# Optimization experiments

Measured on AMD Instinct MI355X. Metric: run time of the kernel, lower is better.

## Reference

```python
import jax, jax.numpy as jnp
import numpy as np

NUM_HEADS = 32  # head_dim = input_dim // num_heads = 32 == C (forced by matmul contraction)


def setup_inputs() -> dict:
    key = jax.random.key(0)
    ks = jax.random.split(key, 8)
    B, C, D3, H1 = 16, 32, 1, 32
    input_dim = 1024  # == C**2, forced by the final view(B, C, H1, W1)
    s = 0.02
    x1 = jax.random.normal(ks[0], (B, C, D3, H1, input_dim), jnp.float32)
    x2 = jax.random.normal(ks[1], (B, C, D3, H1, input_dim), jnp.float32)
    Wq = jax.random.normal(ks[2], (input_dim, input_dim), jnp.float32) * s
    bq = jax.random.normal(ks[3], (input_dim,), jnp.float32) * s
    Wk = jax.random.normal(ks[4], (input_dim, input_dim), jnp.float32) * s
    bk = jax.random.normal(ks[5], (input_dim,), jnp.float32) * s
    Wv = jax.random.normal(ks[6], (input_dim, input_dim), jnp.float32) * s
    bv = jax.random.normal(ks[7], (input_dim,), jnp.float32) * s
    return {"x1": x1, "x2": x2, "Wq": Wq, "bq": bq, "Wk": Wk, "bk": bk, "Wv": Wv, "bv": bv}


def reference(x1, x2, Wq, bq, Wk, bk, Wv, bv):
    B, C, _, H1, W1 = x1.shape  # W1 == input_dim (Linear acts on last dim)
    nh = NUM_HEADS
    hd = W1 // nh
    # Linear projections on the last axis (torch Linear: x @ W.T + b)
    q = (x1 @ Wq.T + bq).reshape(B, C, nh, hd, -1).transpose(0, 2, 4, 3, 1)  # (B, nh, L1, hd, C)
    k = (x2 @ Wk.T + bk).reshape(B, C, nh, hd, -1)                            # (B, C, nh, hd, L2)
    v = (x2 @ Wv.T + bv).reshape(B, C, nh, hd, -1)                            # (B, C, nh, hd, L2)
    # Broadcasted batched matmul: contracts q's trailing C axis with k's hd axis (C == hd).
    energy = jnp.matmul(q, k)                      # (B, C, L1, hd, L2)
    attention = jax.nn.softmax(energy, axis=-1)    # softmax over L2
    # Contracts v's L2 axis with attention's hd axis (L2 == hd).
    out = jnp.matmul(v, attention)                 # (B, C, L1, hd, L2)
    out = out.transpose(0, 2, 4, 3, 1).reshape(B, C, H1, W1)
    return out
```

## Files before the change

kernel.cpp:

```cpp
#include <hip/hip_runtime.h>
#include <cstdint>

typedef __bf16 bf16x8 __attribute__((ext_vector_type(8)));
typedef float f32x4 __attribute__((ext_vector_type(4)));
typedef unsigned short us8 __attribute__((ext_vector_type(8)));

__device__ __forceinline__ unsigned short f2bf(float f) {
  union { float f; uint32_t u; } c; c.f = f;
  uint32_t u = c.u + 0x7FFFu + ((c.u >> 16) & 1u);
  return (unsigned short)(u >> 16);
}
__device__ __forceinline__ float bf2f(unsigned short u) {
  union { uint32_t u; float f; } c; c.u = ((uint32_t)u) << 16; return c.f;
}

__global__ __launch_bounds__(256) void cvt5(
    const float* __restrict__ x1, const float* __restrict__ x2,
    const float* __restrict__ Wq, const float* __restrict__ Wk, const float* __restrict__ Wv,
    unsigned short* __restrict__ xb1, unsigned short* __restrict__ xb2,
    unsigned short* __restrict__ wb) {
  int z = blockIdx.y;
  const float* src; unsigned short* dst; int n4;
  if (z == 0)      { src = x1; dst = xb1;            n4 = 16777216 / 4; }
  else if (z == 1) { src = x2; dst = xb2;            n4 = 16777216 / 4; }
  else if (z == 2) { src = Wq; dst = wb;             n4 = 1048576 / 4; }
  else if (z == 3) { src = Wk; dst = wb + 1048576;   n4 = 1048576 / 4; }
  else             { src = Wv; dst = wb + 2*1048576; n4 = 1048576 / 4; }
  for (int i = blockIdx.x * 256 + threadIdx.x; i < n4; i += gridDim.x * 256) {
    float4 v = ((const float4*)src)[i];
    ushort4 o;
    o.x = f2bf(v.x); o.y = f2bf(v.y); o.z = f2bf(v.z); o.w = f2bf(v.w);
    ((ushort4*)dst)[i] = o;
  }
}

__device__ __forceinline__ void stage_half(const unsigned short* __restrict__ g,
                                           unsigned short* l, int wv, int rl, int cg) {
#pragma unroll
  for (int ld = 0; ld < 2; ++ld) {
    const int chunk = wv * 2 + ld;
    const unsigned short* gp = g + (chunk * 8 + rl) * 1024 + cg * 8;
    unsigned short* lp = l + chunk * 512;
    __builtin_amdgcn_global_load_lds((const __attribute__((address_space(1))) void*)gp,
                                     (__attribute__((address_space(3))) void*)lp,
                                     16, 0, 0);
  }
}

__global__ __launch_bounds__(512) void gemm_qkv(
    const unsigned short* __restrict__ xb1, const unsigned short* __restrict__ xb2,
    const unsigned short* __restrict__ wb,
    const float* __restrict__ bq, const float* __restrict__ bk, const float* __restrict__ bv,
    unsigned short* __restrict__ qkv) {
  __shared__ __attribute__((aligned(16))) unsigned short sm[65536];
  unsigned short* lA0 = sm;
  unsigned short* lB0 = sm + 16384;
  unsigned short* lA1 = sm + 32768;
  unsigned short* lB1 = sm + 49152;

  const int id = blockIdx.x;
  const int swz = (id & 7) * 96 + (id >> 3);
  const int z = swz >> 8;
  const int rem = swz & 255;
  const int mb = rem >> 2;
  const int nb = rem & 3;
  const int m0 = mb * 256;
  const int n0 = nb * 256;

  const unsigned short* Ag = (z == 0) ? xb1 : xb2;
  const unsigned short* Wg = wb + z * 1048576;
  const float* bias = (z == 0) ? bq : (z == 1 ? bk : bv);
  unsigned short* C = qkv + z * 16777216;

  const int tid = threadIdx.x;
  const int lane = tid & 63;
  const int wv = tid >> 6;
  const int wm = wv >> 2;
  const int wn = wv & 3;
  const int mr = lane & 15;
  const int quad = lane >> 4;

  const int rl = lane >> 3;
  const int cg = (lane & 7) ^ rl;

  const int sg0 = ((quad) ^ (mr & 7)) * 8;
  const int sg1 = ((4 + quad) ^ (mr & 7)) * 8;
  const int arow = (wm * 128 + mr) * 64;
  const int brow = (wn * 64 + mr) * 64;

  f32x4 acc[8][4];
#pragma unroll
  for (int i = 0; i < 8; ++i)
#pragma unroll
    for (int j = 0; j < 4; ++j) acc[i][j] = (f32x4){0.f, 0.f, 0.f, 0.f};

  bf16x8 af[4][2], bfr[4][2];

  auto STA = [&](unsigned short* dst, int kt) {
    const unsigned short* g = Ag + m0 * 1024 + kt * 64;
    stage_half(g, dst, wv, rl, cg);
    stage_half(g + 128 * 1024, dst + 8192, wv, rl, cg);
  };
  auto STB = [&](unsigned short* dst, int kt) {
    const unsigned short* g = Wg + n0 * 1024 + kt * 64;
    stage_half(g, dst, wv, rl, cg);
    stage_half(g + 128 * 1024, dst + 8192, wv, rl, cg);
  };
  auto RDA = [&](const unsigned short* lA, int ib) {
#pragma unroll
    for (int i = 0; i < 4; ++i) {
      af[i][0] = *(const bf16x8*)(lA + arow + (ib + i) * 1024 + sg0);
      af[i][1] = *(const bf16x8*)(lA + arow + (ib + i) * 1024 + sg1);
    }
  };
  auto RDB = [&](const unsigned short* lB, int jb) {
#pragma unroll
    for (int j = 0; j < 2; ++j) {
      bfr[jb + j][0] = *(const bf16x8*)(lB + brow + (jb + j) * 1024 + sg0);
      bfr[jb + j][1] = *(const bf16x8*)(lB + brow + (jb + j) * 1024 + sg1);
    }
  };
  auto MF = [&](int ib, int jb) {
#pragma unroll
    for (int i = 0; i < 4; ++i)
#pragma unroll
      for (int j = 0; j < 2; ++j)
#pragma unroll
        for (int h = 0; h < 2; ++h)
          acc[ib + i][jb + j] = __builtin_amdgcn_mfma_f32_16x16x32_bf16(
              af[i][h], bfr[jb + j][h], acc[ib + i][jb + j], 0, 0, 0);
  };

  STA(lA0, 0);
  STB(lB0, 0);
  STA(lA1, 1);
  asm volatile("s_waitcnt vmcnt(4)" ::: "memory");
  __builtin_amdgcn_s_barrier();

#pragma unroll 1
  for (int t = 0; t < 8; ++t) {
    const bool lastt = (t == 7);
    RDA(lA0, 0); RDB(lB0, 0);
    STB(lB1, 2 * t + 1);
    __builtin_amdgcn_s_barrier();
    __builtin_amdgcn_s_setprio(1); MF(0, 0); __builtin_amdgcn_s_setprio(0);
    __builtin_amdgcn_s_barrier();
    RDB(lB0, 2);
    __builtin_amdgcn_s_barrier();
    __builtin_amdgcn_s_setprio(1); MF(0, 2); __builtin_amdgcn_s_setprio(0);
    __builtin_amdgcn_s_barrier();
    RDA(lA0, 4);
    __builtin_amdgcn_s_barrier();
    __builtin_amdgcn_s_setprio(1); MF(4, 0); __builtin_amdgcn_s_setprio(0);
    __builtin_amdgcn_s_barrier();
    if (!lastt) STA(lA0, 2 * t + 2);
    __builtin_amdgcn_s_barrier();
    __builtin_amdgcn_s_setprio(1); MF(4, 2); __builtin_amdgcn_s_setprio(0);
    if (lastt) { asm volatile("s_waitcnt vmcnt(0)" ::: "memory"); }
    else       { asm volatile("s_waitcnt vmcnt(4)" ::: "memory"); }
    __builtin_amdgcn_s_barrier();
    RDA(lA1, 0); RDB(lB1, 0);
    if (!lastt) STB(lB0, 2 * t + 2);
    __builtin_amdgcn_s_barrier();
    __builtin_amdgcn_s_setprio(1); MF(0, 0); __builtin_amdgcn_s_setprio(0);
    __builtin_amdgcn_s_barrier();
    RDB(lB1, 2);
    __builtin_amdgcn_s_barrier();
    __builtin_amdgcn_s_setprio(1); MF(0, 2); __builtin_amdgcn_s_setprio(0);
    __builtin_amdgcn_s_barrier();
    RDA(lA1, 4);
    __builtin_amdgcn_s_barrier();
    __builtin_amdgcn_s_setprio(1); MF(4, 0); __builtin_amdgcn_s_setprio(0);
    __builtin_amdgcn_s_barrier();
    if (!lastt) STA(lA1, 2 * t + 3);
    __builtin_amdgcn_s_barrier();
    __builtin_amdgcn_s_setprio(1); MF(4, 2); __builtin_amdgcn_s_setprio(0);
    if (!lastt) { asm volatile("s_waitcnt vmcnt(4)" ::: "memory"); }
    __builtin_amdgcn_s_barrier();
  }

  {
    unsigned short* strip = sm + wv * 8192;
    float bb[4];
#pragma unroll
    for (int j = 0; j < 4; ++j) bb[j] = bias[n0 + wn * 64 + j * 16 + mr];
#pragma unroll
    for (int i = 0; i < 8; ++i)
#pragma unroll
      for (int j = 0; j < 4; ++j)
#pragma unroll
        for (int r = 0; r < 4; ++r) {
          int row = i * 16 + quad * 4 + r;
          int byteoff = (row * 128 + j * 32 + mr * 2) ^ (((row >> 2) & 3) << 5);
          *(unsigned short*)((char*)strip + byteoff) = f2bf(acc[i][j][r] + bb[j]);
        }
    const int r8 = lane >> 3, c8 = lane & 7;
#pragma unroll
    for (int it = 0; it < 16; ++it) {
      int row = it * 8 + r8;
      int byteoff = (row * 128 + c8 * 16) ^ (((row >> 2) & 3) << 5);
      uint4 vv = *(const uint4*)((const char*)strip + byteoff);
      *(uint4*)(C + (m0 + wm * 128 + row) * 1024 + n0 + wn * 64 + c8 * 8) = vv;
    }
  }
}

__global__ __launch_bounds__(256) void attn(const unsigned short* __restrict__ qkv,
                                            unsigned short* __restrict__ obuf) {
  const unsigned short* qbuf = qkv;
  const unsigned short* kbuf = qkv + 16777216;
  const unsigned short* vbuf = qkv + 2 * 16777216;
  __shared__ __attribute__((aligned(16))) unsigned short qs[8192];
  __shared__ __attribute__((aligned(16))) unsigned short ks[4][1024];
  __shared__ __attribute__((aligned(16))) unsigned short vs[4][1024];
  __shared__ __attribute__((aligned(16))) unsigned short ats[4][1280];
  __shared__ __attribute__((aligned(16))) unsigned short obb[4][1024];
  const int id = blockIdx.x;
  const int xcd = id & 7;
  const int pos = id >> 3;
  const int y0 = (pos & 3) * 8;
  const int bx = (pos >> 2) * 8 + xcd;
  const int b = bx >> 5;
  const int x = bx & 31;
  const int lane = threadIdx.x & 63;
  const int wv = threadIdx.x >> 6;
  const int mr = lane & 15, quad = lane >> 4;

#pragma unroll
  for (int it = 0; it < 4; ++it) {
    int c = threadIdx.x + 256 * it;
    int t = c >> 5, m = c & 31;
    const uint4* src = (const uint4*)(qbuf + ((b * 1024 + t * 32 + x) * 1024 + m * 32 + y0));
    ((uint4*)qs)[c] = *src;
  }
  __syncthreads();

  for (int s = 0; s < 2; ++s) {
    int y = y0 + wv * 2 + s;
    int dy = wv * 2 + s;
    const unsigned short* krow = kbuf + ((b * 32 + x) * 32 + y) * 1024;
    const unsigned short* vrow = vbuf + ((b * 32 + x) * 32 + y) * 1024;
    ((uint4*)ks[wv])[lane] = ((const uint4*)krow)[lane];
    ((uint4*)ks[wv])[64 + lane] = ((const uint4*)krow)[64 + lane];
    ((uint4*)vs[wv])[lane] = ((const uint4*)vrow)[lane];
    ((uint4*)vs[wv])[64 + lane] = ((const uint4*)vrow)[64 + lane];

    bf16x8 qa[2], kb[2];
#pragma unroll
    for (int mt = 0; mt < 2; ++mt) {
      us8 tmp;
#pragma unroll
      for (int jj = 0; jj < 8; ++jj)
        tmp[jj] = qs[((quad * 8 + jj) * 32 + mt * 16 + mr) * 8 + dy];
      qa[mt] = __builtin_bit_cast(bf16x8, tmp);
    }
#pragma unroll
    for (int lt = 0; lt < 2; ++lt) {
      us8 tmp;
#pragma unroll
      for (int jj = 0; jj < 8; ++jj)
        tmp[jj] = ks[wv][(quad * 8 + jj) * 32 + lt * 16 + mr];
      kb[lt] = __builtin_bit_cast(bf16x8, tmp);
    }
    f32x4 e[2][2];
#pragma unroll
    for (int mt = 0; mt < 2; ++mt)
#pragma unroll
      for (int lt = 0; lt < 2; ++lt) {
        f32x4 zz = (f32x4){0.f, 0.f, 0.f, 0.f};
        e[mt][lt] = __builtin_amdgcn_mfma_f32_16x16x32_bf16(qa[mt], kb[lt], zz, 0, 0, 0);
      }

#pragma unroll
    for (int mt = 0; mt < 2; ++mt)
#pragma unroll
      for (int r = 0; r < 4; ++r) {
        float v0 = e[mt][0][r], v1 = e[mt][1][r];
        float mx = fmaxf(v0, v1);
#pragma unroll
        for (int off = 1; off < 16; off <<= 1) mx = fmaxf(mx, __shfl_xor(mx, off));
        float p0 = __expf(v0 - mx), p1 = __expf(v1 - mx);
        float sm = p0 + p1;
#pragma unroll
        for (int off = 1; off < 16; off <<= 1) sm += __shfl_xor(sm, off);
        float inv = 1.0f / sm;
        p0 *= inv; p1 *= inv;
        int trow = mt * 16 + quad * 4 + r;
        ats[wv][mr * 40 + trow] = f2bf(p0);
        ats[wv][(16 + mr) * 40 + trow] = f2bf(p1);
      }

    bf16x8 va[2], pb[2];
#pragma unroll
    for (int i = 0; i < 2; ++i)
      va[i] = *(const bf16x8*)(&vs[wv][(i * 16 + mr) * 32 + quad * 8]);
#pragma unroll
    for (int lt = 0; lt < 2; ++lt)
      pb[lt] = *(const bf16x8*)(&ats[wv][(lt * 16 + mr) * 40 + quad * 8]);
    f32x4 o[2][2];
#pragma unroll
    for (int i = 0; i < 2; ++i)
#pragma unroll
      for (int lt = 0; lt < 2; ++lt) {
        f32x4 zz = (f32x4){0.f, 0.f, 0.f, 0.f};
        o[i][lt] = __builtin_amdgcn_mfma_f32_16x16x32_bf16(va[i], pb[lt], zz, 0, 0, 0);
      }

#pragma unroll
    for (int i = 0; i < 2; ++i)
#pragma unroll
      for (int lt = 0; lt < 2; ++lt)
#pragma unroll
        for (int r = 0; r < 4; ++r)
          obb[wv][(i * 16 + quad * 4 + r) * 32 + lt * 16 + mr] = f2bf(o[i][lt][r]);
    unsigned short* orow = obuf + ((b * 32 + x) * 32 + y) * 1024;
#pragma unroll
    for (int h = 0; h < 2; ++h)
      *(uint4*)(orow + h * 512 + lane * 8) = *(const uint4*)(&obb[wv][h * 512 + lane * 8]);
  }
}

__global__ __launch_bounds__(256) void transpose2(const unsigned short* __restrict__ obuf,
                                                  float* __restrict__ out) {
  __shared__ float t[2][32][36];
  const int y = blockIdx.y, b = blockIdx.z;
  const int r = threadIdx.x >> 3;
  const int cg = threadIdx.x & 7;
  for (int mi = 0; mi < 8; ++mi) {
    int m = blockIdx.x * 8 + mi;
    int buf = mi & 1;
    ushort4 v = *(const ushort4*)(obuf + ((b * 32 + r) * 32 + y) * 1024 + m * 32 + cg * 4);
    t[buf][r][cg * 4 + 0] = bf2f(v.x);
    t[buf][r][cg * 4 + 1] = bf2f(v.y);
    t[buf][r][cg * 4 + 2] = bf2f(v.z);
    t[buf][r][cg * 4 + 3] = bf2f(v.w);
    __syncthreads();
    float4 w;
    w.x = t[buf][cg * 4 + 0][r];
    w.y = t[buf][cg * 4 + 1][r];
    w.z = t[buf][cg * 4 + 2][r];
    w.w = t[buf][cg * 4 + 3][r];
    *(float4*)(out + ((b * 32 + y) * 32 + r) * 1024 + m * 32 + cg * 4) = w;
  }
}

extern "C" void kernel_launch(void* const* d_in, const int* in_sizes, int n_in,
                              void* d_out, int out_size, void* d_ws, size_t ws_size,
                              hipStream_t stream) {
  const float* x1 = (const float*)d_in[0];
  const float* x2 = (const float*)d_in[1];
  const float* Wq = (const float*)d_in[2];
  const float* bq = (const float*)d_in[3];
  const float* Wk = (const float*)d_in[4];
  const float* bk = (const float*)d_in[5];
  const float* Wv = (const float*)d_in[6];
  const float* bv = (const float*)d_in[7];
  float* out = (float*)d_out;

  char* ws = (char*)d_ws;
  unsigned short* xb1 = (unsigned short*)ws;
  unsigned short* xb2 = xb1 + 16777216;
  unsigned short* wb = xb2 + 16777216;
  unsigned short* qkv = wb + 3 * 1048576;
  unsigned short* obuf16 = (unsigned short*)ws;

  cvt5<<<dim3(2048, 5), 256, 0, stream>>>(x1, x2, Wq, Wk, Wv, xb1, xb2, wb);
  gemm_qkv<<<dim3(768), 512, 0, stream>>>(xb1, xb2, wb, bq, bk, bv, qkv);
  attn<<<dim3(2048), 256, 0, stream>>>(qkv, obuf16);
  transpose2<<<dim3(4, 32, 16), 256, 0, stream>>>(obuf16, out);
}
```

Baseline: 330.2 us.

## Permute K weight rows so attention loads K/V fragments directly from global

```diff
diff --git a/kernel.cpp b/kernel.cpp
--- a/kernel.cpp
+++ b/kernel.cpp
@@ -34,19 +34,6 @@
   }
 }
 
-__device__ __forceinline__ void stage_half(const unsigned short* __restrict__ g,
-                                           unsigned short* l, int wv, int rl, int cg) {
-#pragma unroll
-  for (int ld = 0; ld < 2; ++ld) {
-    const int chunk = wv * 2 + ld;
-    const unsigned short* gp = g + (chunk * 8 + rl) * 1024 + cg * 8;
-    unsigned short* lp = l + chunk * 512;
-    __builtin_amdgcn_global_load_lds((const __attribute__((address_space(1))) void*)gp,
-                                     (__attribute__((address_space(3))) void*)lp,
-                                     16, 0, 0);
-  }
-}
-
 __global__ __launch_bounds__(512) void gemm_qkv(
     const unsigned short* __restrict__ xb1, const unsigned short* __restrict__ xb2,
     const unsigned short* __restrict__ wb,
@@ -83,6 +70,22 @@
   const int rl = lane >> 3;
   const int cg = (lane & 7) ^ rl;
 
+  const unsigned short* aptr[4];
+  const unsigned short* bptr[4];
+  int ldoff[4];
+#pragma unroll
+  for (int half = 0; half < 2; ++half)
+#pragma unroll
+    for (int ld = 0; ld < 2; ++ld) {
+      const int q2 = half * 2 + ld;
+      const int chunk = wv * 2 + ld;
+      const int rt = half * 128 + chunk * 8 + rl;
+      aptr[q2] = Ag + (m0 + rt) * 1024 + cg * 8;
+      const int wrow = (z == 1) ? ((rt & 31) * 32 + nb * 8 + (rt >> 5)) : (n0 + rt);
+      bptr[q2] = Wg + wrow * 1024 + cg * 8;
+      ldoff[q2] = half * 8192 + chunk * 512;
+    }
+
   const int sg0 = ((quad) ^ (mr & 7)) * 8;
   const int sg1 = ((4 + quad) ^ (mr & 7)) * 8;
   const int arow = (wm * 128 + mr) * 64;
@@ -97,14 +100,18 @@
   bf16x8 af[4][2], bfr[4][2];
 
   auto STA = [&](unsigned short* dst, int kt) {
-    const unsigned short* g = Ag + m0 * 1024 + kt * 64;
-    stage_half(g, dst, wv, rl, cg);
-    stage_half(g + 128 * 1024, dst + 8192, wv, rl, cg);
+#pragma unroll
+    for (int q2 = 0; q2 < 4; ++q2)
+      __builtin_amdgcn_global_load_lds(
+          (const __attribute__((address_space(1))) void*)(aptr[q2] + kt * 64),
+          (__attribute__((address_space(3))) void*)(dst + ldoff[q2]), 16, 0, 0);
   };
   auto STB = [&](unsigned short* dst, int kt) {
-    const unsigned short* g = Wg + n0 * 1024 + kt * 64;
-    stage_half(g, dst, wv, rl, cg);
-    stage_half(g + 128 * 1024, dst + 8192, wv, rl, cg);
+#pragma unroll
+    for (int q2 = 0; q2 < 4; ++q2)
+      __builtin_amdgcn_global_load_lds(
+          (const __attribute__((address_space(1))) void*)(bptr[q2] + kt * 64),
+          (__attribute__((address_space(3))) void*)(dst + ldoff[q2]), 16, 0, 0);
   };
   auto RDA = [&](const unsigned short* lA, int ib) {
 #pragma unroll
@@ -183,7 +190,11 @@
     unsigned short* strip = sm + wv * 8192;
     float bb[4];
 #pragma unroll
-    for (int j = 0; j < 4; ++j) bb[j] = bias[n0 + wn * 64 + j * 16 + mr];
+    for (int j = 0; j < 4; ++j) {
+      int colp = n0 + wn * 64 + j * 16 + mr;
+      int col = (z == 1) ? ((colp & 31) * 32 + (colp >> 5)) : colp;
+      bb[j] = bias[col];
+    }
 #pragma unroll
     for (int i = 0; i < 8; ++i)
 #pragma unroll
@@ -211,8 +222,6 @@
   const unsigned short* kbuf = qkv + 16777216;
   const unsigned short* vbuf = qkv + 2 * 16777216;
   __shared__ __attribute__((aligned(16))) unsigned short qs[8192];
-  __shared__ __attribute__((aligned(16))) unsigned short ks[4][1024];
-  __shared__ __attribute__((aligned(16))) unsigned short vs[4][1024];
   __shared__ __attribute__((aligned(16))) unsigned short ats[4][1280];
   __shared__ __attribute__((aligned(16))) unsigned short obb[4][1024];
   const int id = blockIdx.x;
@@ -226,42 +235,45 @@
   const int wv = threadIdx.x >> 6;
   const int mr = lane & 15, quad = lane >> 4;
 
+  uint4 kpre[2][2], vpre[2][2];
+#pragma unroll
+  for (int s = 0; s < 2; ++s) {
+    int y = y0 + wv * 2 + s;
+    const unsigned short* krow = kbuf + ((b * 32 + x) * 32 + y) * 1024;
+    const unsigned short* vrow = vbuf + ((b * 32 + x) * 32 + y) * 1024;
+#pragma unroll
+    for (int lt = 0; lt < 2; ++lt)
+      kpre[s][lt] = *(const uint4*)(krow + (lt * 16 + mr) * 32 + quad * 8);
+#pragma unroll
+    for (int i = 0; i < 2; ++i)
+      vpre[s][i] = *(const uint4*)(vrow + (i * 16 + mr) * 32 + quad * 8);
+  }
+
 #pragma unroll
   for (int it = 0; it < 4; ++it) {
-    int c = threadIdx.x + 256 * it;
-    int t = c >> 5, m = c & 31;
-    const uint4* src = (const uint4*)(qbuf + ((b * 1024 + t * 32 + x) * 1024 + m * 32 + y0));
-    ((uint4*)qs)[c] = *src;
+    int cl = threadIdx.x + 256 * it;
+    int t = cl >> 5, m = cl & 31;
+    uint4 v = *(const uint4*)(qbuf + ((b * 1024 + t * 32 + x) * 1024 + m * 32 + y0));
+    us8 e = __builtin_bit_cast(us8, v);
+    int g = ((t >> 3) ^ ((m >> 1) & 3)) * 8 + (t & 7);
+#pragma unroll
+    for (int dy = 0; dy < 8; ++dy)
+      qs[dy * 1024 + m * 32 + g] = e[dy];
   }
   __syncthreads();
 
   for (int s = 0; s < 2; ++s) {
     int y = y0 + wv * 2 + s;
     int dy = wv * 2 + s;
-    const unsigned short* krow = kbuf + ((b * 32 + x) * 32 + y) * 1024;
-    const unsigned short* vrow = vbuf + ((b * 32 + x) * 32 + y) * 1024;
-    ((uint4*)ks[wv])[lane] = ((const uint4*)krow)[lane];
-    ((uint4*)ks[wv])[64 + lane] = ((const uint4*)krow)[64 + lane];
-    ((uint4*)vs[wv])[lane] = ((const uint4*)vrow)[lane];
-    ((uint4*)vs[wv])[64 + lane] = ((const uint4*)vrow)[64 + lane];
 
     bf16x8 qa[2], kb[2];
 #pragma unroll
-    for (int mt = 0; mt < 2; ++mt) {
-      us8 tmp;
-#pragma unroll
-      for (int jj = 0; jj < 8; ++jj)
-        tmp[jj] = qs[((quad * 8 + jj) * 32 + mt * 16 + mr) * 8 + dy];
-      qa[mt] = __builtin_bit_cast(bf16x8, tmp);
-    }
-#pragma unroll
-    for (int lt = 0; lt < 2; ++lt) {
-      us8 tmp;
-#pragma unroll
-      for (int jj = 0; jj < 8; ++jj)
-        tmp[jj] = ks[wv][(quad * 8 + jj) * 32 + lt * 16 + mr];
-      kb[lt] = __builtin_bit_cast(bf16x8, tmp);
-    }
+    for (int mt = 0; mt < 2; ++mt)
+      qa[mt] = *(const bf16x8*)(qs + dy * 1024 + (mt * 16 + mr) * 32 +
+                                (quad ^ ((mr >> 1) & 3)) * 8);
+    kb[0] = __builtin_bit_cast(bf16x8, kpre[s][0]);
+    kb[1] = __builtin_bit_cast(bf16x8, kpre[s][1]);
+
     f32x4 e[2][2];
 #pragma unroll
     for (int mt = 0; mt < 2; ++mt)
@@ -291,9 +303,8 @@
       }
 
     bf16x8 va[2], pb[2];
-#pragma unroll
-    for (int i = 0; i < 2; ++i)
-      va[i] = *(const bf16x8*)(&vs[wv][(i * 16 + mr) * 32 + quad * 8]);
+    va[0] = __builtin_bit_cast(bf16x8, vpre[s][0]);
+    va[1] = __builtin_bit_cast(bf16x8, vpre[s][1]);
 #pragma unroll
     for (int lt = 0; lt < 2; ++lt)
       pb[lt] = *(const bf16x8*)(&ats[wv][(lt * 16 + mr) * 40 + quad * 8]);
```

After: 324.9 us. Within noise of the previous version (-1.6%).
